# Kernel optimization log

Measured on AMD Instinct MI355X. Metric: run time of the kernel, lower is better.

## Reference

```python
import jax, jax.numpy as jnp
import numpy as np

N_EMBD = 768
N_HEAD = 12
LN_EPS = 1e-5

def _gelu_tanh(x):
    # 0.5*x*(1+tanh(sqrt(2/pi)*(x+0.044715*x^3)))
    c = 0.7978845608028654
    return 0.5 * x * (1.0 + jnp.tanh(c * (x + 0.044715 * x * x * x)))

def _layernorm(x, g, b):
    mu = jnp.mean(x, axis=-1, keepdims=True)
    var = jnp.mean(jnp.square(x - mu), axis=-1, keepdims=True)
    return (x - mu) * jax.lax.rsqrt(var + LN_EPS) * g + b

def setup_inputs() -> dict:
    key = jax.random.key(0)
    ks = jax.random.split(key, 8)
    C = N_EMBD
    s = 0.02
    return {
        "x": jax.random.normal(ks[0], (4, 2048, C), jnp.float32),
        "ln1_g": jnp.ones((C,), jnp.float32),
        "ln1_b": jnp.zeros((C,), jnp.float32),
        "attn_w": jax.random.normal(ks[1], (3 * C, C), jnp.float32) * s,
        "attn_b": jnp.zeros((3 * C,), jnp.float32),
        "proj_w": jax.random.normal(ks[2], (C, C), jnp.float32) * s,
        "proj_b": jnp.zeros((C,), jnp.float32),
        "ln2_g": jnp.ones((C,), jnp.float32),
        "ln2_b": jnp.zeros((C,), jnp.float32),
        "fc_w": jax.random.normal(ks[3], (4 * C, C), jnp.float32) * s,
        "fc_b": jnp.zeros((4 * C,), jnp.float32),
        "fc2_w": jax.random.normal(ks[4], (C, 4 * C), jnp.float32) * s,
        "fc2_b": jnp.zeros((C,), jnp.float32),
    }

def reference(x, ln1_g, ln1_b, attn_w, attn_b, proj_w, proj_b,
              ln2_g, ln2_b, fc_w, fc_b, fc2_w, fc2_b):
    B, T, C = x.shape
    H = N_HEAD
    D = C // H

    # --- attention branch ---
    h = _layernorm(x, ln1_g, ln1_b)
    qkv = h @ attn_w.T + attn_b            # [B,T,3C]
    q, k, v = jnp.split(qkv, 3, axis=-1)
    q = q.reshape(B, T, H, D).transpose(0, 2, 1, 3)  # [B,H,T,D]
    k = k.reshape(B, T, H, D).transpose(0, 2, 1, 3)
    v = v.reshape(B, T, H, D).transpose(0, 2, 1, 3)

    att = jnp.einsum('bhqd,bhkd->bhqk', q, k) * (1.0 / np.sqrt(D))
    causal = jnp.tril(jnp.ones((T, T), bool))
    att = jnp.where(causal, att, -jnp.inf)
    att = jax.nn.softmax(att, axis=-1)
    y = jnp.einsum('bhqk,bhkd->bhqd', att, v)        # [B,H,T,D]
    y = y.transpose(0, 2, 1, 3).reshape(B, T, C)
    y = y @ proj_w.T + proj_b
    x = x + y

    # --- MLP branch ---
    h2 = _layernorm(x, ln2_g, ln2_b)
    m = _gelu_tanh(h2 @ fc_w.T + fc_b)
    m = m @ fc2_w.T + fc2_b
    return x + m
```

## Files before the change

### kernel.cpp

```cpp
#include <hip/hip_runtime.h>
#include <hip/hip_bf16.h>

#define N_EMBD 768
#define N_HEADS 12
#define HEAD_DIM 64

typedef __attribute__((ext_vector_type(4))) float f32x4;
typedef __attribute__((ext_vector_type(8))) short s16x8;

__device__ __forceinline__ float bf2f(unsigned short u) {
  union { unsigned int i; float f; } z;
  z.i = ((unsigned int)u) << 16;
  return z.f;
}

__device__ __forceinline__ void gload_lds16(const void* g, void* l) {
  __builtin_amdgcn_global_load_lds(
      (const __attribute__((address_space(1))) void*)g,
      (__attribute__((address_space(3))) void*)l, 16, 0, 0);
}

__device__ __forceinline__ float gelu_f(float x) {
  const float c = 0.7978845608028654f;
  float u = c * (x + 0.044715f * x * x * x);
  float t = 1.0f - 2.0f / (__expf(2.0f * u) + 1.0f);
  return 0.5f * x * (1.0f + t);
}

__global__ void cvt4_kernel(const float* __restrict__ s0, __hip_bfloat16* d0,
                            const float* __restrict__ s1, __hip_bfloat16* d1,
                            const float* __restrict__ s2, __hip_bfloat16* d2,
                            const float* __restrict__ s3, __hip_bfloat16* d3,
                            int n0, int n1, int n2, int n3) {
  int i = blockIdx.x * 256 + threadIdx.x;
  if (i < n0) { d0[i] = __float2bfloat16(s0[i]); return; }
  i -= n0;
  if (i < n1) { d1[i] = __float2bfloat16(s1[i]); return; }
  i -= n1;
  if (i < n2) { d2[i] = __float2bfloat16(s2[i]); return; }
  i -= n2;
  if (i < n3) d3[i] = __float2bfloat16(s3[i]);
}

__global__ __launch_bounds__(256) void ln_kernel(
    const float* __restrict__ x, const float* __restrict__ g,
    const float* __restrict__ b, __hip_bfloat16* __restrict__ out) {
  __shared__ float red[8];
  const int row = blockIdx.x;
  const int tid = threadIdx.x;
  const float* xr = x + (size_t)row * N_EMBD;
  float v0 = xr[tid], v1 = xr[tid + 256], v2 = xr[tid + 512];
  float s = v0 + v1 + v2;
#pragma unroll
  for (int m = 32; m >= 1; m >>= 1) s += __shfl_xor(s, m);
  if ((tid & 63) == 0) red[tid >> 6] = s;
  __syncthreads();
  float mu = (red[0] + red[1] + red[2] + red[3]) * (1.0f / 768.0f);
  float d0 = v0 - mu, d1 = v1 - mu, d2 = v2 - mu;
  float ss = d0 * d0 + d1 * d1 + d2 * d2;
  __syncthreads();
#pragma unroll
  for (int m = 32; m >= 1; m >>= 1) ss += __shfl_xor(ss, m);
  if ((tid & 63) == 0) red[4 + (tid >> 6)] = ss;
  __syncthreads();
  float var = (red[4] + red[5] + red[6] + red[7]) * (1.0f / 768.0f);
  float rstd = rsqrtf(var + 1e-5f);
  __hip_bfloat16* orow = out + (size_t)row * N_EMBD;
  orow[tid]       = __float2bfloat16(d0 * rstd * g[tid]       + b[tid]);
  orow[tid + 256] = __float2bfloat16(d1 * rstd * g[tid + 256] + b[tid + 256]);
  orow[tid + 512] = __float2bfloat16(d2 * rstd * g[tid + 512] + b[tid + 512]);
}

#define TILE_M 128
#define TILE_N 128
#define TILE_K 32

template <int EPI>
__global__ __launch_bounds__(256) void gemm_bt(
    const __hip_bfloat16* __restrict__ A, const __hip_bfloat16* __restrict__ W,
    const float* __restrict__ bias, const float* __restrict__ resid,
    __hip_bfloat16* __restrict__ outb, float* __restrict__ outf,
    int M, int N, int K) {
  __shared__ __hip_bfloat16 smA[2][TILE_M * TILE_K];
  __shared__ __hip_bfloat16 smB[2][TILE_N * TILE_K];
  const int tid = threadIdx.x;
  const int lane = tid & 63;
  const int wave = tid >> 6;

  const int nbx = gridDim.x;
  const int nby = gridDim.y;
  int brow, bcol;
  if ((nby & 3) == 0 && (nbx & 1) == 0) {
    const int b0 = blockIdx.y * nbx + blockIdx.x;
    const int xcd = b0 & 7;
    const int idx = b0 >> 3;
    const int RW = nbx >> 1;
    brow = (xcd >> 1) * (nby >> 2) + idx / RW;
    bcol = (xcd & 1) * RW + idx % RW;
  } else {
    brow = blockIdx.y; bcol = blockIdx.x;
  }
  const int m0 = brow * TILE_M;
  const int n0 = bcol * TILE_N;
  const int wr = wave >> 1, wc = wave & 1;

  f32x4 acc[4][4];
#pragma unroll
  for (int i = 0; i < 4; ++i)
#pragma unroll
    for (int j = 0; j < 4; ++j) acc[i][j] = f32x4{0.f, 0.f, 0.f, 0.f};

  const int ar0 = tid >> 2;
  const int ac0 = (((tid & 3) ^ ((ar0 >> 1) & 3))) * 8;
  const __hip_bfloat16* Abase0 = A + (size_t)(m0 + ar0) * K + ac0;
  const __hip_bfloat16* Abase1 = A + (size_t)(m0 + 64 + ar0) * K + ac0;
  const __hip_bfloat16* Wbase0 = W + (size_t)(n0 + ar0) * K + ac0;
  const __hip_bfloat16* Wbase1 = W + (size_t)(n0 + 64 + ar0) * K + ac0;

  auto stage = [&](int buf, int k0) {
    gload_lds16(Abase0 + k0, &smA[buf][wave * 512]);
    gload_lds16(Abase1 + k0, &smA[buf][2048 + wave * 512]);
    gload_lds16(Wbase0 + k0, &smB[buf][wave * 512]);
    gload_lds16(Wbase1 + k0, &smB[buf][2048 + wave * 512]);
  };

  const int rA = lane & 15;
  const int fq = lane >> 4;
  const int nk = K / TILE_K;

  stage(0, 0);

  int cur = 0;
  for (int t = 0; t < nk; ++t) {
    asm volatile("s_waitcnt vmcnt(0)" ::: "memory");
    asm volatile("s_barrier" ::: "memory");
    if (t + 1 < nk) stage(cur ^ 1, (t + 1) * TILE_K);

    s16x8 af[4], bfr[4];
#pragma unroll
    for (int mi = 0; mi < 4; ++mi) {
      const int row = wr * 64 + mi * 16 + rA;
      const int g = fq ^ ((row >> 1) & 3);
      af[mi] = *(const s16x8*)&smA[cur][row * TILE_K + g * 8];
    }
#pragma unroll
    for (int ni = 0; ni < 4; ++ni) {
      const int row = wc * 64 + ni * 16 + rA;
      const int g = fq ^ ((row >> 1) & 3);
      bfr[ni] = *(const s16x8*)&smB[cur][row * TILE_K + g * 8];
    }
#pragma unroll
    for (int mi = 0; mi < 4; ++mi)
#pragma unroll
      for (int ni = 0; ni < 4; ++ni)
        acc[mi][ni] = __builtin_amdgcn_mfma_f32_16x16x32_bf16(
            af[mi], bfr[ni], acc[mi][ni], 0, 0, 0);
    cur ^= 1;
  }

  const int crow = (lane >> 4) * 4;
  const int ccol = lane & 15;
#pragma unroll
  for (int mi = 0; mi < 4; ++mi) {
#pragma unroll
    for (int ni = 0; ni < 4; ++ni) {
      const int col = n0 + wc * 64 + ni * 16 + ccol;
      const float bv = bias[col];
#pragma unroll
      for (int j = 0; j < 4; ++j) {
        const int row = m0 + wr * 64 + mi * 16 + crow + j;
        float v = acc[mi][ni][j] + bv;
        const size_t o = (size_t)row * N + col;
        if (EPI == 0) {
          outb[o] = __float2bfloat16(v);
        } else if (EPI == 1) {
          outb[o] = __float2bfloat16(gelu_f(v));
        } else {
          outf[o] = resid[o] + v;
        }
      }
    }
  }
}

#define AP 72

__global__ __launch_bounds__(256) void attn_mfma(
    const __hip_bfloat16* __restrict__ qkv, __hip_bfloat16* __restrict__ y,
    int T) {
  __shared__ __hip_bfloat16 ks[2][64 * AP];
  __shared__ __hip_bfloat16 vt[2][64 * AP];
  __shared__ __hip_bfloat16 ps[4][16 * AP];
  const int tid = threadIdx.x;
  const int lane = tid & 63;
  const int wave = tid >> 6;

  const int nbx = gridDim.x;
  const int nwg = nbx * gridDim.y;
  int bid = blockIdx.y * nbx + blockIdx.x;
  if ((nwg & 7) == 0) bid = (bid & 7) * (nwg >> 3) + (bid >> 3);
  const int bx = bid % nbx;
  const int bh = bid / nbx;
  const int b = bh / N_HEADS, h = bh % N_HEADS;

  const int nq = T / 64;
  const int qa0 = bx * 64;
  const int qb0 = (nq - 1 - bx) * 64;
  const size_t ldq = 3 * N_EMBD;
  const __hip_bfloat16* qb_ = qkv + (size_t)b * T * ldq + h * HEAD_DIM;
  const __hip_bfloat16* kb = qb_ + N_EMBD;
  const __hip_bfloat16* vb = qb_ + 2 * N_EMBD;

  const int fr = lane & 15;
  const int fo = (lane >> 4) * 8;
  const int crow = (lane >> 4) * 4;

  const float qs = 0.125f * 1.44269504f;
  auto loadq = [&](int qrow, int o) -> s16x8 {
    s16x8 v = *(const s16x8*)(qb_ + (size_t)qrow * ldq + o);
    s16x8 r;
#pragma unroll
    for (int i = 0; i < 8; ++i) {
      float f = bf2f((unsigned short)v[i]) * qs;
      __hip_bfloat16 hb = __float2bfloat16(f);
      r[i] = *reinterpret_cast<short*>(&hb);
    }
    return r;
  };
  s16x8 qfa0 = loadq(qa0 + wave * 16 + fr, fo);
  s16x8 qfa1 = loadq(qa0 + wave * 16 + fr, fo + 32);
  s16x8 qfb0 = loadq(qb0 + wave * 16 + fr, fo);
  s16x8 qfb1 = loadq(qb0 + wave * 16 + fr, fo + 32);

  f32x4 oa[4], ob[4];
#pragma unroll
  for (int j = 0; j < 4; ++j) {
    oa[j] = f32x4{0.f, 0.f, 0.f, 0.f};
    ob[j] = f32x4{0.f, 0.f, 0.f, 0.f};
  }
  float m_a = -1e30f, l_a = 0.f, m_b = -1e30f, l_b = 0.f;

  s16x8 kr0, kr1, vr0, vr1;
  const int krow0 = tid >> 3;
  const int kcol = (tid & 7) * 8;
  const int vkey = 2 * (lane & 31);
  const int vd0 = wave * 16 + (lane >> 5) * 8;

  auto loadKV = [&](int kt) {
    kr0 = *(const s16x8*)(kb + (size_t)(kt + krow0) * ldq + kcol);
    kr1 = *(const s16x8*)(kb + (size_t)(kt + 32 + krow0) * ldq + kcol);
    vr0 = *(const s16x8*)(vb + (size_t)(kt + vkey) * ldq + vd0);
    vr1 = *(const s16x8*)(vb + (size_t)(kt + vkey + 1) * ldq + vd0);
  };
  auto writeKV = [&](int bufi) {
    *(s16x8*)&ks[bufi][krow0 * AP + kcol] = kr0;
    *(s16x8*)&ks[bufi][(32 + krow0) * AP + kcol] = kr1;
#pragma unroll
    for (int i = 0; i < 8; ++i) {
      unsigned u = (unsigned short)vr0[i] | ((unsigned)(unsigned short)vr1[i] << 16);
      *(unsigned*)&vt[bufi][(vd0 + i) * AP + vkey] = u;
    }
  };

  auto process = [&](int bufi, const s16x8& q0f, const s16x8& q1f,
                     f32x4 (&o)[4], float& m_, float& l_, int tq0, bool diag,
                     int kt) {
    f32x4 sv[4];
#pragma unroll
    for (int sub = 0; sub < 4; ++sub) {
      s16x8 k0 = *(const s16x8*)&ks[bufi][(sub * 16 + fr) * AP + fo];
      s16x8 k1 = *(const s16x8*)&ks[bufi][(sub * 16 + fr) * AP + 32 + fo];
      f32x4 acc = f32x4{0.f, 0.f, 0.f, 0.f};
      acc = __builtin_amdgcn_mfma_f32_16x16x32_bf16(k0, q0f, acc, 0, 0, 0);
      acc = __builtin_amdgcn_mfma_f32_16x16x32_bf16(k1, q1f, acc, 0, 0, 0);
      sv[sub] = acc;
    }
    const int qg = tq0 + wave * 16 + fr;
    if (diag) {
#pragma unroll
      for (int sub = 0; sub < 4; ++sub)
#pragma unroll
        for (int j = 0; j < 4; ++j)
          if (kt + sub * 16 + crow + j > qg) sv[sub][j] = -1e30f;
    }
    float g0 = fmaxf(fmaxf(sv[0][0], sv[0][1]), fmaxf(sv[0][2], sv[0][3]));
    float g1 = fmaxf(fmaxf(sv[1][0], sv[1][1]), fmaxf(sv[1][2], sv[1][3]));
    float g2 = fmaxf(fmaxf(sv[2][0], sv[2][1]), fmaxf(sv[2][2], sv[2][3]));
    float g3 = fmaxf(fmaxf(sv[3][0], sv[3][1]), fmaxf(sv[3][2], sv[3][3]));
    float t = fmaxf(fmaxf(g0, g1), fmaxf(g2, g3));
    t = fmaxf(t, __shfl_xor(t, 16));
    t = fmaxf(t, __shfl_xor(t, 32));
    const bool resc = t > m_ + 8.0f;
    const float corr = resc ? exp2f(m_ - t) : 1.0f;
    if (resc) m_ = t;
    float rs = 0.f;
#pragma unroll
    for (int sub = 0; sub < 4; ++sub) {
      float p0 = exp2f(sv[sub][0] - m_);
      float p1 = exp2f(sv[sub][1] - m_);
      float p2 = exp2f(sv[sub][2] - m_);
      float p3 = exp2f(sv[sub][3] - m_);
      rs += (p0 + p1) + (p2 + p3);
      __hip_bfloat162 pk01 = __float22bfloat162_rn(float2{p0, p1});
      __hip_bfloat162 pk23 = __float22bfloat162_rn(float2{p2, p3});
      uint2 u;
      u.x = *reinterpret_cast<unsigned*>(&pk01);
      u.y = *reinterpret_cast<unsigned*>(&pk23);
      *(uint2*)&ps[wave][fr * AP + sub * 16 + crow] = u;
    }
    rs += __shfl_xor(rs, 16);
    rs += __shfl_xor(rs, 32);
    l_ = l_ * corr + rs;
    if (__any(resc)) {
#pragma unroll
      for (int j = 0; j < 4; ++j) {
        const float cj = __shfl(corr, (lane & 0x30) | (crow + j));
#pragma unroll
        for (int ds = 0; ds < 4; ++ds) o[ds][j] *= cj;
      }
    }
    s16x8 pf0 = *(const s16x8*)&ps[wave][fr * AP + fo];
    s16x8 pf1 = *(const s16x8*)&ps[wave][fr * AP + 32 + fo];
#pragma unroll
    for (int ds = 0; ds < 4; ++ds) {
      s16x8 v0 = *(const s16x8*)&vt[bufi][(ds * 16 + fr) * AP + fo];
      s16x8 v1 = *(const s16x8*)&vt[bufi][(ds * 16 + fr) * AP + 32 + fo];
      o[ds] = __builtin_amdgcn_mfma_f32_16x16x32_bf16(pf0, v0, o[ds], 0, 0, 0);
      o[ds] = __builtin_amdgcn_mfma_f32_16x16x32_bf16(pf1, v1, o[ds], 0, 0, 0);
    }
  };

  loadKV(0);
  writeKV(0);
  __syncthreads();
  int cur = 0;
  for (int kt = 0; kt <= qb0; kt += 64) {
    const bool hasnext = (kt + 64 <= qb0);
    if (hasnext) loadKV(kt + 64);
    if (kt <= qa0)
      process(cur, qfa0, qfa1, oa, m_a, l_a, qa0, kt == qa0, kt);
    process(cur, qfb0, qfb1, ob, m_b, l_b, qb0, kt == qb0, kt);
    if (hasnext) writeKV(cur ^ 1);
    __syncthreads();
    cur ^= 1;
  }

#pragma unroll
  for (int j = 0; j < 4; ++j) {
    const float la_j = __shfl(l_a, (lane & 0x30) | (crow + j));
    const float lb_j = __shfl(l_b, (lane & 0x30) | (crow + j));
    const float inva = 1.0f / la_j;
    const float invb = 1.0f / lb_j;
    __hip_bfloat16* ya =
        y + (size_t)(b * T + qa0 + wave * 16 + crow + j) * N_EMBD + h * HEAD_DIM;
    __hip_bfloat16* yb =
        y + (size_t)(b * T + qb0 + wave * 16 + crow + j) * N_EMBD + h * HEAD_DIM;
#pragma unroll
    for (int ds = 0; ds < 4; ++ds) {
      ya[ds * 16 + fr] = __float2bfloat16(oa[ds][j] * inva);
      yb[ds * 16 + fr] = __float2bfloat16(ob[ds][j] * invb);
    }
  }
}

extern "C" void kernel_launch(void* const* d_in, const int* in_sizes, int n_in,
                              void* d_out, int out_size, void* d_ws,
                              size_t ws_size, hipStream_t stream) {
  const int B = 4, T = 2048, C = N_EMBD;
  const int M = B * T;

  const float* x      = (const float*)d_in[0];
  const float* ln1_g  = (const float*)d_in[1];
  const float* ln1_b  = (const float*)d_in[2];
  const float* attn_w = (const float*)d_in[3];
  const float* attn_b = (const float*)d_in[4];
  const float* proj_w = (const float*)d_in[5];
  const float* proj_b = (const float*)d_in[6];
  const float* ln2_g  = (const float*)d_in[7];
  const float* ln2_b  = (const float*)d_in[8];
  const float* fc_w   = (const float*)d_in[9];
  const float* fc_b   = (const float*)d_in[10];
  const float* fc2_w  = (const float*)d_in[11];
  const float* fc2_b  = (const float*)d_in[12];
  float* out = (float*)d_out;

  char* p = (char*)d_ws;
  size_t off = 0;
  auto take = [&](size_t bytes) -> void* {
    void* q = p + off;
    off += (bytes + 1023) & ~(size_t)1023;
    return q;
  };

  __hip_bfloat16* wqkv  = (__hip_bfloat16*)take((size_t)3 * C * C * 2);
  __hip_bfloat16* wproj = (__hip_bfloat16*)take((size_t)C * C * 2);
  __hip_bfloat16* wfc   = (__hip_bfloat16*)take((size_t)4 * C * C * 2);
  __hip_bfloat16* wfc2  = (__hip_bfloat16*)take((size_t)4 * C * C * 2);
  __hip_bfloat16* hbuf  = (__hip_bfloat16*)take((size_t)M * C * 2);
  __hip_bfloat16* big   = (__hip_bfloat16*)take((size_t)M * 4 * C * 2);
  __hip_bfloat16* ybuf  = (__hip_bfloat16*)take((size_t)M * C * 2);
  float*          x1    = (float*)take((size_t)M * C * 4);

  {
    const int n0 = 3 * C * C, n1 = C * C, n2 = 4 * C * C, n3 = 4 * C * C;
    const int ntot = n0 + n1 + n2 + n3;
    cvt4_kernel<<<(ntot + 255) / 256, 256, 0, stream>>>(
        attn_w, wqkv, proj_w, wproj, fc_w, wfc, fc2_w, wfc2, n0, n1, n2, n3);
  }

  ln_kernel<<<M, 256, 0, stream>>>(x, ln1_g, ln1_b, hbuf);
  gemm_bt<0><<<dim3(3 * C / TILE_N, M / TILE_M), 256, 0, stream>>>(
      hbuf, wqkv, attn_b, nullptr, big, nullptr, M, 3 * C, C);
  attn_mfma<<<dim3(T / 128, B * N_HEADS), 256, 0, stream>>>(big, ybuf, T);
  gemm_bt<2><<<dim3(C / TILE_N, M / TILE_M), 256, 0, stream>>>(
      ybuf, wproj, proj_b, x, nullptr, x1, M, C, C);
  ln_kernel<<<M, 256, 0, stream>>>(x1, ln2_g, ln2_b, hbuf);
  gemm_bt<1><<<dim3(4 * C / TILE_N, M / TILE_M), 256, 0, stream>>>(
      hbuf, wfc, fc_b, nullptr, big, nullptr, M, 4 * C, C);
  gemm_bt<2><<<dim3(C / TILE_N, M / TILE_M), 256, 0, stream>>>(
      big, wfc2, fc2_b, x1, nullptr, out, M, C, 4 * C);
}
```

Before: 292.1 us.

## Replace LDS-staged GEMM with direct global-to-register MFMA operand loads

The GEMM kernel no longer stages A and W tiles through shared memory with barriers. Each wave loads its MFMA fragments straight from global memory into registers, double-buffered across K steps, so the LDS traffic and block-wide synchronisation go away. The cost is that the two waves sharing a row or column of the tile each load the same data, and each lane's 16-byte loads are strided by K, which risks poorer coalescing and more reliance on the L1/L2 caches.

```diff
diff --git a/kernel.cpp b/kernel.cpp
--- a/kernel.cpp
+++ b/kernel.cpp
@@ -73,22 +73,18 @@
 
 #define TILE_M 128
 #define TILE_N 128
-#define TILE_K 32
 
 template <int EPI>
-__global__ __launch_bounds__(256) void gemm_bt(
+__global__ __launch_bounds__(256) void gemm_reg(
     const __hip_bfloat16* __restrict__ A, const __hip_bfloat16* __restrict__ W,
     const float* __restrict__ bias, const float* __restrict__ resid,
     __hip_bfloat16* __restrict__ outb, float* __restrict__ outf,
     int M, int N, int K) {
-  __shared__ __hip_bfloat16 smA[2][TILE_M * TILE_K];
-  __shared__ __hip_bfloat16 smB[2][TILE_N * TILE_K];
   const int tid = threadIdx.x;
   const int lane = tid & 63;
   const int wave = tid >> 6;
 
-  const int nbx = gridDim.x;
-  const int nby = gridDim.y;
+  const int nbx = gridDim.x, nby = gridDim.y;
   int brow, bcol;
   if ((nby & 3) == 0 && (nbx & 1) == 0) {
     const int b0 = blockIdx.y * nbx + blockIdx.x;
@@ -103,6 +99,8 @@
   const int m0 = brow * TILE_M;
   const int n0 = bcol * TILE_N;
   const int wr = wave >> 1, wc = wave & 1;
+  const int fr = lane & 15;
+  const int fq = lane >> 4;
 
   f32x4 acc[4][4];
 #pragma unroll
@@ -110,56 +108,42 @@
 #pragma unroll
     for (int j = 0; j < 4; ++j) acc[i][j] = f32x4{0.f, 0.f, 0.f, 0.f};
 
-  const int ar0 = tid >> 2;
-  const int ac0 = (((tid & 3) ^ ((ar0 >> 1) & 3))) * 8;
-  const __hip_bfloat16* Abase0 = A + (size_t)(m0 + ar0) * K + ac0;
-  const __hip_bfloat16* Abase1 = A + (size_t)(m0 + 64 + ar0) * K + ac0;
-  const __hip_bfloat16* Wbase0 = W + (size_t)(n0 + ar0) * K + ac0;
-  const __hip_bfloat16* Wbase1 = W + (size_t)(n0 + 64 + ar0) * K + ac0;
-
-  auto stage = [&](int buf, int k0) {
-    gload_lds16(Abase0 + k0, &smA[buf][wave * 512]);
-    gload_lds16(Abase1 + k0, &smA[buf][2048 + wave * 512]);
-    gload_lds16(Wbase0 + k0, &smB[buf][wave * 512]);
-    gload_lds16(Wbase1 + k0, &smB[buf][2048 + wave * 512]);
-  };
-
-  const int rA = lane & 15;
-  const int fq = lane >> 4;
-  const int nk = K / TILE_K;
-
-  stage(0, 0);
-
-  int cur = 0;
-  for (int t = 0; t < nk; ++t) {
-    asm volatile("s_waitcnt vmcnt(0)" ::: "memory");
-    asm volatile("s_barrier" ::: "memory");
-    if (t + 1 < nk) stage(cur ^ 1, (t + 1) * TILE_K);
-
-    s16x8 af[4], bfr[4];
-#pragma unroll
-    for (int mi = 0; mi < 4; ++mi) {
-      const int row = wr * 64 + mi * 16 + rA;
-      const int g = fq ^ ((row >> 1) & 3);
-      af[mi] = *(const s16x8*)&smA[cur][row * TILE_K + g * 8];
-    }
-#pragma unroll
-    for (int ni = 0; ni < 4; ++ni) {
-      const int row = wc * 64 + ni * 16 + rA;
-      const int g = fq ^ ((row >> 1) & 3);
-      bfr[ni] = *(const s16x8*)&smB[cur][row * TILE_K + g * 8];
-    }
+  const __hip_bfloat16* Ab[4];
+  const __hip_bfloat16* Wb[4];
+#pragma unroll
+  for (int i = 0; i < 4; ++i) {
+    Ab[i] = A + (size_t)(m0 + wr * 64 + i * 16 + fr) * K + fq * 8;
+    Wb[i] = W + (size_t)(n0 + wc * 64 + i * 16 + fr) * K + fq * 8;
+  }
+
+  const int nk = K / 32;
+  s16x8 a0[4], b0[4], a1[4], b1[4];
+
+  auto ld = [&](s16x8 (&af)[4], s16x8 (&bf_)[4], int k0) {
+#pragma unroll
+    for (int i = 0; i < 4; ++i) af[i] = *(const s16x8*)(Ab[i] + k0);
+#pragma unroll
+    for (int i = 0; i < 4; ++i) bf_[i] = *(const s16x8*)(Wb[i] + k0);
+  };
+  auto mm = [&](s16x8 (&af)[4], s16x8 (&bf_)[4]) {
 #pragma unroll
     for (int mi = 0; mi < 4; ++mi)
 #pragma unroll
       for (int ni = 0; ni < 4; ++ni)
         acc[mi][ni] = __builtin_amdgcn_mfma_f32_16x16x32_bf16(
-            af[mi], bfr[ni], acc[mi][ni], 0, 0, 0);
-    cur ^= 1;
-  }
-
-  const int crow = (lane >> 4) * 4;
-  const int ccol = lane & 15;
+            af[mi], bf_[ni], acc[mi][ni], 0, 0, 0);
+  };
+
+  ld(a0, b0, 0);
+  for (int t = 0; t < nk; t += 2) {
+    if (t + 1 < nk) ld(a1, b1, (t + 1) * 32);
+    mm(a0, b0);
+    if (t + 2 < nk) ld(a0, b0, (t + 2) * 32);
+    if (t + 1 < nk) mm(a1, b1);
+  }
+
+  const int crow = fq * 4;
+  const int ccol = fr;
 #pragma unroll
   for (int mi = 0; mi < 4; ++mi) {
 #pragma unroll
@@ -409,14 +393,14 @@
   }
 
   ln_kernel<<<M, 256, 0, stream>>>(x, ln1_g, ln1_b, hbuf);
-  gemm_bt<0><<<dim3(3 * C / TILE_N, M / TILE_M), 256, 0, stream>>>(
+  gemm_reg<0><<<dim3(3 * C / TILE_N, M / TILE_M), 256, 0, stream>>>(
       hbuf, wqkv, attn_b, nullptr, big, nullptr, M, 3 * C, C);
   attn_mfma<<<dim3(T / 128, B * N_HEADS), 256, 0, stream>>>(big, ybuf, T);
-  gemm_bt<2><<<dim3(C / TILE_N, M / TILE_M), 256, 0, stream>>>(
+  gemm_reg<2><<<dim3(C / TILE_N, M / TILE_M), 256, 0, stream>>>(
       ybuf, wproj, proj_b, x, nullptr, x1, M, C, C);
   ln_kernel<<<M, 256, 0, stream>>>(x1, ln2_g, ln2_b, hbuf);
-  gemm_bt<1><<<dim3(4 * C / TILE_N, M / TILE_M), 256, 0, stream>>>(
+  gemm_reg<1><<<dim3(4 * C / TILE_N, M / TILE_M), 256, 0, stream>>>(
       hbuf, wfc, fc_b, nullptr, big, nullptr, M, 4 * C, C);
-  gemm_bt<2><<<dim3(C / TILE_N, M / TILE_M), 256, 0, stream>>>(
+  gemm_reg<2><<<dim3(C / TILE_N, M / TILE_M), 256, 0, stream>>>(
       big, wfc2, fc2_b, x1, nullptr, out, M, C, 4 * C);
 }
```

After: 569.2 us. +94.8%, slower.
